# Performance work log

Measured on AMD Instinct MI355X. Metric: run time of the kernel, lower is better.

The kernel has to match this reference:

```python
import jax, jax.numpy as jnp
import numpy as np

DIM = 1024
DEPTH = 4
D_STATE = 16
D_CONV = 4
D_INNER = 2 * DIM
DT_RANK = (DIM + 15) // 16  # 64, ceil(dim/16) as in mamba-ssm
B_SZ, L = 4, 2048


def setup_inputs() -> dict:
    key = jax.random.key(0)
    ks = jax.random.split(key, 10)
    s = 0.02
    x = jax.random.normal(ks[0], (B_SZ, L, DIM), jnp.float32)
    in_proj_w = jax.random.normal(ks[1], (DEPTH, 2 * D_INNER, DIM), jnp.float32) * s
    conv_w = jax.random.normal(ks[2], (DEPTH, D_INNER, D_CONV), jnp.float32) * 0.2
    conv_b = jnp.zeros((DEPTH, D_INNER), jnp.float32)
    x_proj_w = jax.random.normal(ks[3], (DEPTH, DT_RANK + 2 * D_STATE, D_INNER), jnp.float32) * s
    dt_proj_w = jax.random.normal(ks[4], (DEPTH, D_INNER, DT_RANK), jnp.float32) * s
    # bias init so softplus(bias) ~ 0.01 (mamba dt_init)
    dt_proj_b = jnp.full((DEPTH, D_INNER), float(np.log(np.expm1(0.01))), jnp.float32)
    # S4D-real init: A = -(1..d_state)
    A_log = jnp.broadcast_to(jnp.log(jnp.arange(1, D_STATE + 1, dtype=jnp.float32)), (D_INNER, D_STATE))
    A_log = jnp.broadcast_to(A_log, (DEPTH, D_INNER, D_STATE))
    D = jnp.ones((DEPTH, D_INNER), jnp.float32)
    out_proj_w = jax.random.normal(ks[5], (DEPTH, DIM, D_INNER), jnp.float32) * s
    return {"x": x, "in_proj_w": in_proj_w, "conv_w": conv_w, "conv_b": conv_b,
            "x_proj_w": x_proj_w, "dt_proj_w": dt_proj_w, "dt_proj_b": dt_proj_b,
            "A_log": A_log, "D": D, "out_proj_w": out_proj_w}


def _selective_scan(u, delta, A, Bm, Cm, D):
    # u, delta: [B, L, d_inner]; Bm, Cm: [B, L, d_state]; A: [d_inner, d_state]
    def step(h, inp):
        u_t, d_t, b_t, c_t = inp  # [B,di], [B,di], [B,ds], [B,ds]
        dA = jnp.exp(d_t[:, :, None] * A)                 # [B,di,ds]
        h = dA * h + (d_t * u_t)[:, :, None] * b_t[:, None, :]
        y = jnp.einsum('bds,bs->bd', h, c_t)
        return h, y

    h0 = jnp.zeros((u.shape[0], u.shape[2], A.shape[1]), u.dtype)
    xs = (u.transpose(1, 0, 2), delta.transpose(1, 0, 2),
          Bm.transpose(1, 0, 2), Cm.transpose(1, 0, 2))
    _, ys = jax.lax.scan(step, h0, xs)                     # ys: [L,B,di]
    return ys.transpose(1, 0, 2) + u * D


def _mamba_layer(x, in_w, cw, cb, xp_w, dtw, dtb, A_log, D, ow):
    xz = jnp.einsum('bld,ed->ble', x, in_w)               # [B,L,2*di]
    xi, z = jnp.split(xz, 2, axis=-1)
    # causal depthwise conv over L
    xc = jax.lax.conv_general_dilated(
        xi.transpose(0, 2, 1),                             # [B,di,L]
        cw[:, None, :],                                    # [di,1,k]
        window_strides=(1,), padding=[(D_CONV - 1, 0)],
        feature_group_count=D_INNER,
        dimension_numbers=('NCH', 'OIH', 'NCH'))
    xc = jax.nn.silu(xc.transpose(0, 2, 1) + cb)           # [B,L,di]
    dbc = jnp.einsum('bld,ed->ble', xc, xp_w)              # [B,L,dt_rank+2*ds]
    dt, Bm, Cm = jnp.split(dbc, [DT_RANK, DT_RANK + D_STATE], axis=-1)
    delta = jax.nn.softplus(jnp.einsum('blr,dr->bld', dt, dtw) + dtb)
    A = -jnp.exp(A_log)
    y = _selective_scan(xc, delta, A, Bm, Cm, D)
    y = y * jax.nn.silu(z)
    return jnp.einsum('bld,od->blo', y, ow)


def reference(x, in_proj_w, conv_w, conv_b, x_proj_w, dt_proj_w, dt_proj_b, A_log, D, out_proj_w):
    for i in range(DEPTH):
        x = _mamba_layer(x, in_proj_w[i], conv_w[i], conv_b[i], x_proj_w[i],
                         dt_proj_w[i], dt_proj_b[i], A_log[i], D[i], out_proj_w[i])
    return x
```

## Files before the change

kernel.cpp:

```cpp
#include <hip/hip_runtime.h>
#include <hip/hip_bf16.h>
#include <math.h>

#define DIMK 1024
#define NDEPTH 4
#define DS 16
#define DCONV 4
#define DI 2048
#define DTR 64
#define NB 4
#define SL 2048
#define MT (NB * SL)
#define NXZ (2 * DI)
#define NDBC (DTR + 2 * DS)

typedef float f32x4 __attribute__((ext_vector_type(4)));
typedef short short8 __attribute__((ext_vector_type(8)));
typedef short short4v __attribute__((ext_vector_type(4)));

__device__ inline unsigned short f2bf(float f) {
    unsigned u = __builtin_bit_cast(unsigned, f);
    unsigned r = (u + 0x7FFFu + ((u >> 16) & 1u)) >> 16;
    return (unsigned short)r;
}
__device__ inline float bf2f(unsigned short h) {
    unsigned u = ((unsigned)h) << 16;
    return __builtin_bit_cast(float, u);
}
__device__ inline void split_bf(float f, unsigned short& hi, unsigned short& lo) {
    hi = f2bf(f);
    lo = f2bf(f - bf2f(hi));
}
__device__ inline unsigned short cvt1(float f) {
    __hip_bfloat16 t = __float2bfloat16(f);
    return __builtin_bit_cast(unsigned short, t);
}
__device__ inline void mfma16(f32x4& d, short8 a, short8 b) {
    asm volatile("v_mfma_f32_16x16x32_bf16 %0, %1, %2, %0"
                 : "+v"(d) : "v"(a), "v"(b));
}
__device__ __forceinline__ float dpp_sum16(float p) {
    asm("v_add_f32_dpp %0, %0, %0 quad_perm:[1,0,3,2] row_mask:0xf bank_mask:0xf bound_ctrl:0" : "+v"(p));
    asm("v_add_f32_dpp %0, %0, %0 quad_perm:[2,3,0,1] row_mask:0xf bank_mask:0xf bound_ctrl:0" : "+v"(p));
    asm("v_add_f32_dpp %0, %0, %0 row_ror:4 row_mask:0xf bank_mask:0xf bound_ctrl:0" : "+v"(p));
    asm("v_add_f32_dpp %0, %0, %0 row_ror:8 row_mask:0xf bank_mask:0xf bound_ctrl:0" : "+v"(p));
    return p;
}
__device__ __forceinline__ float exp2_raw(float x) {
    float r;
    asm("v_exp_f32 %0, %1" : "=v"(r) : "v"(x));
    return r;
}
__device__ __forceinline__ void gload16(const unsigned short* g, unsigned short* l) {
    __builtin_amdgcn_global_load_lds(
        (const __attribute__((address_space(1))) unsigned int*)(g),
        (__attribute__((address_space(3))) unsigned int*)(l),
        16, 0, 0);
}

__global__ __launch_bounds__(256) void cvt_bf16(
    const float* __restrict__ s, unsigned short* __restrict__ d, int n4)
{
    const int g = blockIdx.x * 256 + threadIdx.x;
    if (g < n4) {
        const float4 f = *(const float4*)(s + (size_t)g * 4);
        short4v v;
        v[0] = (short)cvt1(f.x); v[1] = (short)cvt1(f.y);
        v[2] = (short)cvt1(f.z); v[3] = (short)cvt1(f.w);
        *(short4v*)(d + (size_t)g * 4) = v;
    }
}

__global__ __launch_bounds__(256) void cvt_layer(
    const float* __restrict__ wi, const float* __restrict__ owp,
    const float* __restrict__ dtwp, const float* __restrict__ xpwp,
    unsigned short* __restrict__ wi16, unsigned short* __restrict__ ow16,
    unsigned short* __restrict__ dtwh, unsigned short* __restrict__ dtwl,
    unsigned short* __restrict__ xpwh, unsigned short* __restrict__ xpwl,
    int fastd, int fastx)
{
    int g = blockIdx.x * 256 + threadIdx.x;
    const int n4w = NXZ * DIMK / 4;
    const int n4o = DIMK * DI / 4;
    const int n4d = DI * DTR / 4;
    const int n4x = NDBC * DI / 4;
    if (g < n4w) {
        const float4 f = *(const float4*)(wi + (size_t)g * 4);
        short4v v;
        v[0] = (short)cvt1(f.x); v[1] = (short)cvt1(f.y);
        v[2] = (short)cvt1(f.z); v[3] = (short)cvt1(f.w);
        *(short4v*)(wi16 + (size_t)g * 4) = v;
        return;
    }
    g -= n4w;
    if (g < n4o) {
        const float4 f = *(const float4*)(owp + (size_t)g * 4);
        short4v v;
        v[0] = (short)cvt1(f.x); v[1] = (short)cvt1(f.y);
        v[2] = (short)cvt1(f.z); v[3] = (short)cvt1(f.w);
        *(short4v*)(ow16 + (size_t)g * 4) = v;
        return;
    }
    g -= n4o;
    if (g < n4d) {
        if (fastd) {
            const float4 f = *(const float4*)(dtwp + (size_t)g * 4);
            short4v h4, l4;
            #pragma unroll
            for (int e = 0; e < 4; ++e) {
                unsigned short h, l;
                split_bf((&f.x)[e], h, l);
                h4[e] = (short)h; l4[e] = (short)l;
            }
            *(short4v*)(dtwh + (size_t)g * 4) = h4;
            *(short4v*)(dtwl + (size_t)g * 4) = l4;
        }
        return;
    }
    g -= n4d;
    if (g < n4x && fastx) {
        const float4 f = *(const float4*)(xpwp + (size_t)g * 4);
        short4v h4, l4;
        #pragma unroll
        for (int e = 0; e < 4; ++e) {
            unsigned short h, l;
            split_bf((&f.x)[e], h, l);
            h4[e] = (short)h; l4[e] = (short)l;
        }
        *(short4v*)(xpwh + (size_t)g * 4) = h4;
        *(short4v*)(xpwl + (size_t)g * 4) = l4;
    }
}

template <int CBF>
__global__ __launch_bounds__(256) void gemm_bb(
    const unsigned short* __restrict__ A, const unsigned short* __restrict__ B,
    void* __restrict__ Cv, int K, int lda, int ldb, int ldc)
{
    __shared__ unsigned short As[2][128 * 32];
    __shared__ unsigned short Bs[2][128 * 32];
    int id = blockIdx.y * gridDim.x + blockIdx.x;
    const int qq = (gridDim.x * gridDim.y) >> 3;
    id = (id & 7) * qq + (id >> 3);
    const int bm = (id / gridDim.x) * 128, bn = (id % gridDim.x) * 128;

    const int tid = threadIdx.x;
    const int wv = tid >> 6, ln = tid & 63;
    const int wr = wv >> 1, wc = wv & 1;
    const int fr = ln & 15, kg = ln >> 4;
    const int sr0 = wv * 32 + (ln >> 2);
    const int sr1 = sr0 + 16;
    const int sl = ln & 3;
    const int cg0 = sl ^ ((sr0 >> 1) & 3);
    const int cg1 = sl ^ ((sr1 >> 1) & 3);
    const unsigned short* pa0 = A + (size_t)(bm + sr0) * lda + cg0 * 8;
    const unsigned short* pa1 = A + (size_t)(bm + sr1) * lda + cg1 * 8;
    const unsigned short* pb0 = B + (size_t)(bn + sr0) * ldb + cg0 * 8;
    const unsigned short* pb1 = B + (size_t)(bn + sr1) * ldb + cg1 * 8;
    const int ldst0 = (wv * 32 + 0) * 32;
    const int ldst1 = (wv * 32 + 16) * 32;
    int offA[4], offB[4];
    #pragma unroll
    for (int f = 0; f < 4; ++f) {
        const int ra = wr * 64 + f * 16 + fr;
        offA[f] = ra * 32 + ((kg ^ ((ra >> 1) & 3)) * 8);
        const int rb = wc * 64 + f * 16 + fr;
        offB[f] = rb * 32 + ((kg ^ ((rb >> 1) & 3)) * 8);
    }
    f32x4 acc[4][4] = {};
    gload16(pa0, &As[0][ldst0]);
    gload16(pa1, &As[0][ldst1]);
    gload16(pb0, &Bs[0][ldst0]);
    gload16(pb1, &Bs[0][ldst1]);
    __syncthreads();
    int cur = 0;
    for (int k0 = 0; k0 < K; k0 += 32) {
        const int nxt = cur ^ 1;
        if (k0 + 32 < K) {
            gload16(pa0 + k0 + 32, &As[nxt][ldst0]);
            gload16(pa1 + k0 + 32, &As[nxt][ldst1]);
            gload16(pb0 + k0 + 32, &Bs[nxt][ldst0]);
            gload16(pb1 + k0 + 32, &Bs[nxt][ldst1]);
        }
        short8 af[4], bw[4];
        #pragma unroll
        for (int f = 0; f < 4; ++f) {
            af[f] = *(const short8*)&As[cur][offA[f]];
            bw[f] = *(const short8*)&Bs[cur][offB[f]];
        }
        #pragma unroll
        for (int fi = 0; fi < 4; ++fi)
            #pragma unroll
            for (int fj = 0; fj < 4; ++fj)
                mfma16(acc[fi][fj], af[fi], bw[fj]);
        __syncthreads();
        cur = nxt;
    }
    #pragma unroll
    for (int fi = 0; fi < 4; ++fi) {
        const int m0 = bm + wr * 64 + fi * 16 + kg * 4;
        #pragma unroll
        for (int fj = 0; fj < 4; ++fj) {
            const int n = bn + wc * 64 + fj * 16 + fr;
            #pragma unroll
            for (int q = 0; q < 4; ++q) {
                if (CBF) {
                    unsigned short* Cs = (unsigned short*)Cv;
                    Cs[(size_t)(m0 + q) * ldc + n] = cvt1(acc[fi][fj][q]);
                } else {
                    float* Cf = (float*)Cv;
                    Cf[(size_t)(m0 + q) * ldc + n] = acc[fi][fj][q];
                }
            }
        }
    }
}

template <int CBF>
__global__ __launch_bounds__(256) void gemm_fb(
    const float* __restrict__ A, const unsigned short* __restrict__ B,
    void* __restrict__ Cv, int K, int lda, int ldb, int ldc)
{
    __shared__ unsigned short As[2][128 * 32];
    __shared__ unsigned short Bs[2][128 * 32];
    int id = blockIdx.y * gridDim.x + blockIdx.x;
    const int qq = (gridDim.x * gridDim.y) >> 3;
    id = (id & 7) * qq + (id >> 3);
    const int bm = (id / gridDim.x) * 128, bn = (id % gridDim.x) * 128;

    const int tid = threadIdx.x;
    const int wv = tid >> 6, ln = tid & 63;
    const int wr = wv >> 1, wc = wv & 1;
    const int fr = ln & 15, kg = ln >> 4;
    const int r = tid >> 1, hf = tid & 1;
    const int sr0 = wv * 32 + (ln >> 2);
    const int sr1 = sr0 + 16;
    const int sl = ln & 3;
    const int cg0 = sl ^ ((sr0 >> 1) & 3);
    const int cg1 = sl ^ ((sr1 >> 1) & 3);
    const unsigned short* pb0 = B + (size_t)(bn + sr0) * ldb + cg0 * 8;
    const unsigned short* pb1 = B + (size_t)(bn + sr1) * ldb + cg1 * 8;
    const int ldst0 = (wv * 32 + 0) * 32;
    const int ldst1 = (wv * 32 + 16) * 32;
    const float* ga = A + (size_t)(bm + r) * lda + hf * 16;
    const int pk0 = (2 * hf + 0) ^ ((r >> 1) & 3);
    const int pk1 = (2 * hf + 1) ^ ((r >> 1) & 3);
    int offA[4], offB[4];
    #pragma unroll
    for (int f = 0; f < 4; ++f) {
        const int ra = wr * 64 + f * 16 + fr;
        offA[f] = ra * 32 + ((kg ^ ((ra >> 1) & 3)) * 8);
        const int rb = wc * 64 + f * 16 + fr;
        offB[f] = rb * 32 + ((kg ^ ((rb >> 1) & 3)) * 8);
    }
    f32x4 acc[4][4] = {};
    {
        float4 f0 = *(const float4*)(ga + 0);
        float4 f1 = *(const float4*)(ga + 4);
        float4 f2 = *(const float4*)(ga + 8);
        float4 f3 = *(const float4*)(ga + 12);
        short8 v;
        v[0] = (short)cvt1(f0.x); v[1] = (short)cvt1(f0.y);
        v[2] = (short)cvt1(f0.z); v[3] = (short)cvt1(f0.w);
        v[4] = (short)cvt1(f1.x); v[5] = (short)cvt1(f1.y);
        v[6] = (short)cvt1(f1.z); v[7] = (short)cvt1(f1.w);
        *(short8*)&As[0][r * 32 + pk0 * 8] = v;
        v[0] = (short)cvt1(f2.x); v[1] = (short)cvt1(f2.y);
        v[2] = (short)cvt1(f2.z); v[3] = (short)cvt1(f2.w);
        v[4] = (short)cvt1(f3.x); v[5] = (short)cvt1(f3.y);
        v[6] = (short)cvt1(f3.z); v[7] = (short)cvt1(f3.w);
        *(short8*)&As[0][r * 32 + pk1 * 8] = v;
        gload16(pb0, &Bs[0][ldst0]);
        gload16(pb1, &Bs[0][ldst1]);
    }
    __syncthreads();
    int cur = 0;
    for (int k0 = 0; k0 < K; k0 += 32) {
        const int nxt = cur ^ 1;
        const bool more = (k0 + 32 < K);
        float4 f0, f1, f2, f3;
        if (more) {
            gload16(pb0 + k0 + 32, &Bs[nxt][ldst0]);
            gload16(pb1 + k0 + 32, &Bs[nxt][ldst1]);
            f0 = *(const float4*)(ga + k0 + 32);
            f1 = *(const float4*)(ga + k0 + 36);
            f2 = *(const float4*)(ga + k0 + 40);
            f3 = *(const float4*)(ga + k0 + 44);
        }
        short8 af[4], bw[4];
        #pragma unroll
        for (int f = 0; f < 4; ++f) {
            af[f] = *(const short8*)&As[cur][offA[f]];
            bw[f] = *(const short8*)&Bs[cur][offB[f]];
        }
        #pragma unroll
        for (int fi = 0; fi < 4; ++fi)
            #pragma unroll
            for (int fj = 0; fj < 4; ++fj)
                mfma16(acc[fi][fj], af[fi], bw[fj]);
        if (more) {
            short8 v;
            v[0] = (short)cvt1(f0.x); v[1] = (short)cvt1(f0.y);
            v[2] = (short)cvt1(f0.z); v[3] = (short)cvt1(f0.w);
            v[4] = (short)cvt1(f1.x); v[5] = (short)cvt1(f1.y);
            v[6] = (short)cvt1(f1.z); v[7] = (short)cvt1(f1.w);
            *(short8*)&As[nxt][r * 32 + pk0 * 8] = v;
            v[0] = (short)cvt1(f2.x); v[1] = (short)cvt1(f2.y);
            v[2] = (short)cvt1(f2.z); v[3] = (short)cvt1(f2.w);
            v[4] = (short)cvt1(f3.x); v[5] = (short)cvt1(f3.y);
            v[6] = (short)cvt1(f3.z); v[7] = (short)cvt1(f3.w);
            *(short8*)&As[nxt][r * 32 + pk1 * 8] = v;
        }
        __syncthreads();
        cur = nxt;
    }
    #pragma unroll
    for (int fi = 0; fi < 4; ++fi) {
        const int m0 = bm + wr * 64 + fi * 16 + kg * 4;
        #pragma unroll
        for (int fj = 0; fj < 4; ++fj) {
            const int n = bn + wc * 64 + fj * 16 + fr;
            #pragma unroll
            for (int q = 0; q < 4; ++q) {
                if (CBF) {
                    unsigned short* Cs = (unsigned short*)Cv;
                    Cs[(size_t)(m0 + q) * ldc + n] = cvt1(acc[fi][fj][q]);
                } else {
                    float* Cf = (float*)Cv;
                    Cf[(size_t)(m0 + q) * ldc + n] = acc[fi][fj][q];
                }
            }
        }
    }
}

__global__ __launch_bounds__(256) void gemm_mfma(
    const float* __restrict__ A, const float* __restrict__ W,
    float* __restrict__ C, int K, int lda, int ldc)
{
    __shared__ unsigned short As[128 * 32];
    __shared__ unsigned short Ws[128 * 32];
    const int tid = threadIdx.x;
    const int bm = blockIdx.y * 128;
    const int bn = blockIdx.x * 128;
    const int r = tid >> 1;
    const int h = tid & 1;
    const int wv = tid >> 6;
    const int wr = wv >> 1;
    const int wc = wv & 1;
// ... 342 lines not shown
        const int dst = (wv * 32 + j * 8) * 64;
        gload16(Ahg + (size_t)(bm + row) * DTR + scol, sAh + dst);
        gload16(Alg + (size_t)(bm + row) * DTR + scol, sAl + dst);
        gload16(Whg + (size_t)(bn + row) * DTR + scol, sWh + dst);
        gload16(Wlg + (size_t)(bn + row) * DTR + scol, sWl + dst);
    }
    __syncthreads();
    f32x4 acc[4][4] = {};
    #pragma unroll
    for (int ks = 0; ks < 2; ++ks) {
        short8 ah[4], alo[4], bh[4], bl[4];
        #pragma unroll
        for (int f = 0; f < 4; ++f) {
            const int ra = wr * 64 + f * 16 + fr;
            const int ao = ra * 64 + ks * 32 + ((kg ^ ((ra >> 1) & 3)) * 8);
            ah[f]  = *(const short8*)&sAh[ao];
            alo[f] = *(const short8*)&sAl[ao];
            const int rb = wc * 64 + f * 16 + fr;
            const int bo = rb * 64 + ks * 32 + ((kg ^ ((rb >> 1) & 3)) * 8);
            bh[f] = *(const short8*)&sWh[bo];
            bl[f] = *(const short8*)&sWl[bo];
        }
        #pragma unroll
        for (int fi = 0; fi < 4; ++fi)
            #pragma unroll
            for (int fj = 0; fj < 4; ++fj) {
                mfma16(acc[fi][fj], ah[fi], bh[fj]);
                mfma16(acc[fi][fj], ah[fi], bl[fj]);
                mfma16(acc[fi][fj], alo[fi], bh[fj]);
            }
    }
    #pragma unroll
    for (int fi = 0; fi < 4; ++fi) {
        const int m0 = bm + wr * 64 + fi * 16 + kg * 4;
        #pragma unroll
        for (int fj = 0; fj < 4; ++fj) {
            const int n = bn + wc * 64 + fj * 16 + fr;
            const float bb = bias[n];
            #pragma unroll
            for (int q = 0; q < 4; ++q) {
                float v = acc[fi][fj][q] + bb;
                v = (v > 20.f) ? v : log1pf(__expf(v));
                C[(size_t)(m0 + q) * NXZ + n] = v;
            }
        }
    }
}

__global__ __launch_bounds__(256) void conv_silu(
    const float* __restrict__ xz, const float* __restrict__ cw,
    const float* __restrict__ cb, float* __restrict__ xc)
{
    const int g = blockIdx.x * 256 + threadIdx.x;
    const int c4 = g & (DI / 4 - 1);
    const int mq = g >> 9;
    const int m0 = mq << 2;
    const int l0 = m0 & (SL - 1);
    const int c = c4 << 2;
    const float4 w0 = *(const float4*)(cw + (size_t)(c + 0) * DCONV);
    const float4 w1 = *(const float4*)(cw + (size_t)(c + 1) * DCONV);
    const float4 w2 = *(const float4*)(cw + (size_t)(c + 2) * DCONV);
    const float4 w3 = *(const float4*)(cw + (size_t)(c + 3) * DCONV);
    const float4 cb4 = *(const float4*)(cb + c);
    float4 x[7];
    #pragma unroll
    for (int i = 0; i < 7; ++i) {
        if (l0 - 3 + i >= 0)
            x[i] = *(const float4*)(xz + (size_t)(m0 - 3 + i) * NXZ + c);
        else
            x[i] = make_float4(0.f, 0.f, 0.f, 0.f);
    }
    #pragma unroll
    for (int j = 0; j < 4; ++j) {
        float4 acc = cb4;
        #pragma unroll
        for (int k = 0; k < DCONV; ++k) {
            const float4 v = x[j + k];
            acc.x = fmaf(v.x, (&w0.x)[k], acc.x);
            acc.y = fmaf(v.y, (&w1.x)[k], acc.y);
            acc.z = fmaf(v.z, (&w2.x)[k], acc.z);
            acc.w = fmaf(v.w, (&w3.x)[k], acc.w);
        }
        acc.x = acc.x / (1.f + __expf(-acc.x));
        acc.y = acc.y / (1.f + __expf(-acc.y));
        acc.z = acc.z / (1.f + __expf(-acc.z));
        acc.w = acc.w / (1.f + __expf(-acc.w));
        *(float4*)(xc + (size_t)(m0 + j) * DI + c) = acc;
    }
}

__global__ __launch_bounds__(256) void conv_silu_split(
    const float* __restrict__ xz, const float* __restrict__ cw,
    const float* __restrict__ cb, unsigned short* __restrict__ xch,
    unsigned short* __restrict__ xcl)
{
    const int g = blockIdx.x * 256 + threadIdx.x;
    const int c4 = g & (DI / 4 - 1);
    const int mq = g >> 9;
    const int m0 = mq << 2;
    const int l0 = m0 & (SL - 1);
    const int c = c4 << 2;
    const float4 w0 = *(const float4*)(cw + (size_t)(c + 0) * DCONV);
    const float4 w1 = *(const float4*)(cw + (size_t)(c + 1) * DCONV);
    const float4 w2 = *(const float4*)(cw + (size_t)(c + 2) * DCONV);
    const float4 w3 = *(const float4*)(cw + (size_t)(c + 3) * DCONV);
    const float4 cb4 = *(const float4*)(cb + c);
    float4 x[7];
    #pragma unroll
    for (int i = 0; i < 7; ++i) {
        if (l0 - 3 + i >= 0)
            x[i] = *(const float4*)(xz + (size_t)(m0 - 3 + i) * NXZ + c);
        else
            x[i] = make_float4(0.f, 0.f, 0.f, 0.f);
    }
    #pragma unroll
    for (int j = 0; j < 4; ++j) {
        float4 acc = cb4;
        #pragma unroll
        for (int k = 0; k < DCONV; ++k) {
            const float4 v = x[j + k];
            acc.x = fmaf(v.x, (&w0.x)[k], acc.x);
            acc.y = fmaf(v.y, (&w1.x)[k], acc.y);
            acc.z = fmaf(v.z, (&w2.x)[k], acc.z);
            acc.w = fmaf(v.w, (&w3.x)[k], acc.w);
        }
        short4v h4, l4;
        #pragma unroll
        for (int e = 0; e < 4; ++e) {
            float a = (&acc.x)[e];
            a = a / (1.f + __expf(-a));
            unsigned short hh, llo;
            split_bf(a, hh, llo);
            h4[e] = (short)hh; l4[e] = (short)llo;
        }
        *(short4v*)(xch + (size_t)(m0 + j) * DI + c) = h4;
        *(short4v*)(xcl + (size_t)(m0 + j) * DI + c) = l4;
    }
}

template <int YBF, int UBF>
__global__ __launch_bounds__(256) void scan_k(
    const float* uf, const unsigned short* __restrict__ uh,
    const unsigned short* __restrict__ ul,
    const float* __restrict__ dbc,
    const float* __restrict__ xz, void* __restrict__ yv,
    const float* __restrict__ Alog, const float* __restrict__ Dl)
{
    const int b = blockIdx.y;
    const int c0 = blockIdx.x * 16;
    const int tid = threadIdx.x;
    const int ch = tid >> 4;
    const int s = tid & 15;
    const float Aa = -__expf(Alog[(size_t)(c0 + ch) * DS + s]) * 1.44269504088896f;
    __shared__ float sdl[16][68];
    __shared__ float sxb[16][68];
    __shared__ float sbc[32][68];
    __shared__ float sy[2][64][16];
    __shared__ float sD[16];
    if (tid < 16) sD[tid] = Dl[c0 + tid];
    __syncthreads();
    float h = 0.f;
    const int row = tid >> 2;
    const int q = (tid & 3) << 2;
    int pp = 0;
    for (int t0b = 0; t0b < SL; t0b += 64) {
        const size_t mb = (size_t)b * SL + t0b;
        const float4 dlv = *(const float4*)(xz + (mb + row) * NXZ + c0 + q);
        float4 uv;
        if (UBF) {
            const short4v uh4 = *(const short4v*)(uh + (mb + row) * DI + c0 + q);
            const short4v ul4 = *(const short4v*)(ul + (mb + row) * DI + c0 + q);
            #pragma unroll
            for (int e = 0; e < 4; ++e)
                (&uv.x)[e] = bf2f((unsigned short)uh4[e]) +
                             bf2f((unsigned short)ul4[e]);
        } else {
            uv = *(const float4*)(uf + (mb + row) * DI + c0 + q);
        }
        const float4 zv = *(const float4*)(xz + (mb + row) * NXZ + DI + c0 + q);
        float4 p0, p1;
        #pragma unroll
        for (int j = 0; j < 4; ++j) {
            const float dl = (&dlv.x)[j], uu = (&uv.x)[j], zz = (&zv.x)[j];
            const float w = zz / (1.f + __expf(-zz));
            sdl[q + j][row] = dl;
            sxb[q + j][row] = dl * uu;
            (&p1.x)[j] = w;
            (&p0.x)[j] = uu * sD[q + j] * w;
        }
        #pragma unroll
        for (int p = 0; p < 2; ++p) {
            const int idx = p * 256 + tid;
            const int r2 = idx >> 3, q2 = (idx & 7) << 2;
            const float4 v = *(const float4*)(dbc + (mb + r2) * NDBC + DTR + q2);
            sbc[q2 + 0][r2] = v.x; sbc[q2 + 1][r2] = v.y;
            sbc[q2 + 2][r2] = v.z; sbc[q2 + 3][r2] = v.w;
        }
        __syncthreads();
        for (int it = 0; it < 16; ++it) {
            const int t0 = it * 4;
            const float4 dl4 = *(const float4*)&sdl[ch][t0];
            const float4 xb4 = *(const float4*)&sxb[ch][t0];
            const float4 B4  = *(const float4*)&sbc[s][t0];
            const float4 C4  = *(const float4*)&sbc[16 + s][t0];
            float py0, py1, py2, py3;
            {
                const float dA = exp2_raw(dl4.x * Aa);
                h = fmaf(dA, h, xb4.x * B4.x);
                py0 = dpp_sum16(h * C4.x);
            }
            {
                const float dA = exp2_raw(dl4.y * Aa);
                h = fmaf(dA, h, xb4.y * B4.y);
                py1 = dpp_sum16(h * C4.y);
            }
            {
                const float dA = exp2_raw(dl4.z * Aa);
                h = fmaf(dA, h, xb4.z * B4.z);
                py2 = dpp_sum16(h * C4.z);
            }
            {
                const float dA = exp2_raw(dl4.w * Aa);
                h = fmaf(dA, h, xb4.w * B4.w);
                py3 = dpp_sum16(h * C4.w);
            }
            if (s < 4) {
                const int t = t0 + s;
                const float lo_ = (s & 1) ? py1 : py0;
                const float hi_ = (s & 1) ? py3 : py2;
                sy[pp][t][ch] = (s & 2) ? hi_ : lo_;
            }
        }
        __syncthreads();
        if (YBF) {
            unsigned short* y16 = (unsigned short*)yv;
            short4v s4;
            #pragma unroll
            for (int e = 0; e < 4; ++e)
                s4[e] = (short)cvt1(fmaf(sy[pp][row][q + e],
                                         (&p1.x)[e], (&p0.x)[e]));
            *(short4v*)(y16 + (mb + row) * DI + c0 + q) = s4;
        } else {
            float* y = (float*)yv;
            float4 yvv;
            #pragma unroll
            for (int e = 0; e < 4; ++e)
                (&yvv.x)[e] = fmaf(sy[pp][row][q + e], (&p1.x)[e], (&p0.x)[e]);
            *(float4*)(y + (mb + row) * DI + c0 + q) = yvv;
        }
        pp ^= 1;
    }
}

extern "C" void kernel_launch(void* const* d_in, const int* in_sizes, int n_in,
                              void* d_out, int out_size, void* d_ws, size_t ws_size,
                              hipStream_t stream)
{
    const float* x0   = (const float*)d_in[0];
    const float* in_w = (const float*)d_in[1];
    const float* cw   = (const float*)d_in[2];
    const float* cb   = (const float*)d_in[3];
    const float* xpw  = (const float*)d_in[4];
    const float* dtw  = (const float*)d_in[5];
    const float* dtb  = (const float*)d_in[6];
    const float* Alog = (const float*)d_in[7];
    const float* Dp   = (const float*)d_in[8];
    const float* ow   = (const float*)d_in[9];

    const size_t perB = (size_t)SL * (NXZ + DI + NDBC) * sizeof(float);
    const size_t wby  = ((size_t)NXZ * DIMK + (size_t)DIMK * DI) * 2;
    int nbc = 0, fast = 0;
    if (ws_size >= 4 * perB + wby)      { nbc = 4; fast = 1; }
    else if (ws_size >= 2 * perB + wby) { nbc = 2; fast = 1; }
    else if (ws_size >= perB + wby)     { nbc = 1; fast = 1; }
    else if (ws_size >= 4 * perB)       { nbc = 4; }
    else if (ws_size >= 2 * perB)       { nbc = 2; }
    else if (ws_size >= perB)           { nbc = 1; }
    else return;
    const int nchunks = NB / nbc;
    const int M = nbc * SL;
    const size_t dtby = ((size_t)DI * DTR * 2 + (size_t)M * DTR * 2) * 2;
    const size_t yby  = (size_t)M * DI * 2;
    const size_t xpby = (size_t)NDBC * DI * 2 * 2;
    const size_t base = (size_t)nbc * perB + wby;
    const int fastd = fast && (ws_size >= base + dtby);
    const int fasty = fastd && (ws_size >= base + dtby + yby);
    const int fastx = fasty && (ws_size >= base + dtby + yby + xpby);

    float* xz  = (float*)d_ws;
    float* xc  = xz + (size_t)M * NXZ;
    float* dbc = xc + (size_t)M * DI;
    unsigned short* xch = (unsigned short*)xc;
    unsigned short* xcl = xch + (size_t)M * DI;
    unsigned short* wi16 = (unsigned short*)(dbc + (size_t)M * NDBC);
    unsigned short* ow16 = wi16 + (size_t)NXZ * DIMK;
    unsigned short* dtwh = ow16 + (size_t)DIMK * DI;
    unsigned short* dtwl = dtwh + (size_t)DI * DTR;
    unsigned short* dth  = dtwl + (size_t)DI * DTR;
    unsigned short* dtl  = dth + (size_t)M * DTR;
    unsigned short* y16  = dtl + (size_t)M * DTR;
    unsigned short* xpwh = y16 + (size_t)M * DI;
    unsigned short* xpwl = xpwh + (size_t)NDBC * DI;

    unsigned short* xb16 = (unsigned short*)d_out + (size_t)MT * DIMK;
    float* xbuf = (float*)d_out;

    const dim3 blk(256);
    if (fastx) {
        const int n4x = MT * DIMK / 4;
        cvt_bf16<<<dim3(n4x / 256), blk, 0, stream>>>(x0, xb16, n4x);
    }
    const int ncv = (NXZ * DIMK / 4) + (DIMK * DI / 4) + (DI * DTR / 4) +
                    (NDBC * DI / 4);
    for (int ly = 0; ly < NDEPTH; ++ly) {
        const float* Wi   = in_w + (size_t)ly * NXZ * DIMK;
        const float* cwl  = cw   + (size_t)ly * DI * DCONV;
        const float* cbl  = cb   + (size_t)ly * DI;
        const float* xpl  = xpw  + (size_t)ly * NDBC * DI;
        const float* dtwl_ = dtw + (size_t)ly * DI * DTR;
        const float* dtbl = dtb  + (size_t)ly * DI;
        const float* Al   = Alog + (size_t)ly * DI * DS;
        const float* Dl   = Dp   + (size_t)ly * DI;
        const float* owl  = ow   + (size_t)ly * DIMK * DI;

        if (fast)
            cvt_layer<<<dim3((ncv + 255) / 256), blk, 0, stream>>>(
                Wi, owl, dtwl_, xpl, wi16, ow16, dtwh, dtwl, xpwh, xpwl,
                fastd, fastx);

        for (int ck = 0; ck < nchunks; ++ck) {
            if (fastx) {
                const unsigned short* xin16 = xb16 + (size_t)ck * M * DIMK;
                gemm_bb<0><<<dim3(NXZ / 128, M / 128), blk, 0, stream>>>(
                    xin16, wi16, xz, DIMK, DIMK, DIMK, NXZ);
                conv_silu_split<<<dim3(M * (DI / 16) / 256), blk, 0, stream>>>(
                    xz, cwl, cbl, xch, xcl);
                gemm_xproj_pre<<<dim3(3, M / 128), blk, 0, stream>>>(
                    xch, xcl, xpwh, xpwl, dbc, dth, dtl);
                gemm_delta_pre<<<dim3(DI / 128, M / 128), blk, 0, stream>>>(
                    dth, dtl, dtwh, dtwl, xz, dtbl);
                scan_k<1, 1><<<dim3(DI / 16, nbc), blk, 0, stream>>>(
                    nullptr, xch, xcl, dbc, xz, y16, Al, Dl);
                void* dst = (ly < NDEPTH - 1)
                    ? (void*)(xb16 + (size_t)ck * M * DIMK)
                    : (void*)((float*)d_out + (size_t)ck * M * DIMK);
                if (ly < NDEPTH - 1)
                    gemm_bb<1><<<dim3(DIMK / 128, M / 128), blk, 0, stream>>>(
                        y16, ow16, dst, DI, DI, DI, DIMK);
                else
                    gemm_bb<0><<<dim3(DIMK / 128, M / 128), blk, 0, stream>>>(
                        y16, ow16, dst, DI, DI, DI, DIMK);
            } else if (fast) {
                if (ly == 0) {
                    const float* xin = x0 + (size_t)ck * M * DIMK;
                    gemm_fb<0><<<dim3(NXZ / 128, M / 128), blk, 0, stream>>>(
                        xin, wi16, xz, DIMK, DIMK, DIMK, NXZ);
                } else {
                    const unsigned short* xin16 = xb16 + (size_t)ck * M * DIMK;
                    gemm_bb<0><<<dim3(NXZ / 128, M / 128), blk, 0, stream>>>(
                        xin16, wi16, xz, DIMK, DIMK, DIMK, NXZ);
                }
                conv_silu<<<dim3(M * (DI / 16) / 256), blk, 0, stream>>>(
                    xz, cwl, cbl, xc);
                if (fastd) {
                    gemm_xproj<1><<<dim3(3, M / 128), blk, 0, stream>>>(
                        xc, xpl, dbc, DI, DI, dth, dtl);
                    gemm_delta_pre<<<dim3(DI / 128, M / 128), blk, 0, stream>>>(
                        dth, dtl, dtwh, dtwl, xz, dtbl);
                } else {
                    gemm_xproj<0><<<dim3(3, M / 128), blk, 0, stream>>>(
                        xc, xpl, dbc, DI, DI, nullptr, nullptr);
                    gemm_delta<<<dim3(DI / 128, M / 128), blk, 0, stream>>>(
                        dbc, dtwl_, xz, dtbl);
                }
                void* dst = (ly < NDEPTH - 1)
                    ? (void*)(xb16 + (size_t)ck * M * DIMK)
                    : (void*)((float*)d_out + (size_t)ck * M * DIMK);
                if (fasty) {
                    scan_k<1, 0><<<dim3(DI / 16, nbc), blk, 0, stream>>>(
                        xc, nullptr, nullptr, dbc, xz, y16, Al, Dl);
                    if (ly < NDEPTH - 1)
                        gemm_bb<1><<<dim3(DIMK / 128, M / 128), blk, 0, stream>>>(
                            y16, ow16, dst, DI, DI, DI, DIMK);
                    else
                        gemm_bb<0><<<dim3(DIMK / 128, M / 128), blk, 0, stream>>>(
                            y16, ow16, dst, DI, DI, DI, DIMK);
                } else {
                    scan_k<0, 0><<<dim3(DI / 16, nbc), blk, 0, stream>>>(
                        xc, nullptr, nullptr, dbc, xz, xc, Al, Dl);
                    if (ly < NDEPTH - 1)
                        gemm_fb<1><<<dim3(DIMK / 128, M / 128), blk, 0, stream>>>(
                            xc, ow16, dst, DI, DI, DI, DIMK);
                    else
                        gemm_fb<0><<<dim3(DIMK / 128, M / 128), blk, 0, stream>>>(
                            xc, ow16, dst, DI, DI, DI, DIMK);
                }
            } else {
                const float* xin = (ly == 0 ? x0 : xbuf) + (size_t)ck * M * DIMK;
                gemm_mfma<<<dim3(NXZ / 128, M / 128), blk, 0, stream>>>(
                    xin, Wi, xz, DIMK, DIMK, NXZ);
                conv_silu<<<dim3(M * (DI / 16) / 256), blk, 0, stream>>>(
                    xz, cwl, cbl, xc);
                gemm_xproj<0><<<dim3(3, M / 128), blk, 0, stream>>>(
                    xc, xpl, dbc, DI, DI, nullptr, nullptr);
                gemm_delta<<<dim3(DI / 128, M / 128), blk, 0, stream>>>(
                    dbc, dtwl_, xz, dtbl);
                scan_k<0, 0><<<dim3(DI / 16, nbc), blk, 0, stream>>>(
                    xc, nullptr, nullptr, dbc, xz, xc, Al, Dl);
                float* xdst = (ly == NDEPTH - 1 ? (float*)d_out : xbuf) +
                              (size_t)ck * M * DIMK;
                gemm_mfma<<<dim3(DIMK / 128, M / 128), blk, 0, stream>>>(
                    xc, owl, xdst, DI, DI, DIMK);
            }
        }
    }
}
```

Before: 1.650 ms.

## Prefetch scan tiles with double-buffered LDS, batch weight conversion, single-buffer GEMM

The selective-scan kernel now keeps double-buffered shared tiles. It prefetches the next 64-step tile's global loads into registers and defers the previous tile's output write so both overlap the recurrence. The aim is to hide global memory latency in the serial scan. All layers' weights are converted to bf16 in one launch up front when workspace allows, replacing the per-layer conversion kernels. gemm_bb drops its LDS double buffering and loads synchronously each k-step, which halves its shared memory but exposes load latency.

```diff
diff --git a/kernel.cpp b/kernel.cpp
--- a/kernel.cpp
+++ b/kernel.cpp
@@ -132,13 +132,75 @@
     }
 }
 
+__global__ __launch_bounds__(256) void cvt_all(
+    const float* __restrict__ wi, const float* __restrict__ owp,
+    const float* __restrict__ dtwp, const float* __restrict__ xpwp,
+    unsigned short* __restrict__ wi16, unsigned short* __restrict__ ow16,
+    unsigned short* __restrict__ dtwh, unsigned short* __restrict__ dtwl,
+    unsigned short* __restrict__ xpwh, unsigned short* __restrict__ xpwl)
+{
+    const int n4w = NXZ * DIMK / 4;
+    const int n4o = DIMK * DI / 4;
+    const int n4d = DI * DTR / 4;
+    const int n4x = NDBC * DI / 4;
+    const int per = n4w + n4o + n4d + n4x;
+    int g = blockIdx.x * 256 + threadIdx.x;
+    const int ly = g / per;
+    if (ly >= NDEPTH) return;
+    g -= ly * per;
+    if (g < n4w) {
+        const float4 f = *(const float4*)(wi + (size_t)ly * NXZ * DIMK + (size_t)g * 4);
+        short4v v;
+        v[0] = (short)cvt1(f.x); v[1] = (short)cvt1(f.y);
+        v[2] = (short)cvt1(f.z); v[3] = (short)cvt1(f.w);
+        *(short4v*)(wi16 + (size_t)ly * NXZ * DIMK + (size_t)g * 4) = v;
+        return;
+    }
+    g -= n4w;
+    if (g < n4o) {
+        const float4 f = *(const float4*)(owp + (size_t)ly * DIMK * DI + (size_t)g * 4);
+        short4v v;
+        v[0] = (short)cvt1(f.x); v[1] = (short)cvt1(f.y);
+        v[2] = (short)cvt1(f.z); v[3] = (short)cvt1(f.w);
+        *(short4v*)(ow16 + (size_t)ly * DIMK * DI + (size_t)g * 4) = v;
+        return;
+    }
+    g -= n4o;
+    if (g < n4d) {
+        const float4 f = *(const float4*)(dtwp + (size_t)ly * DI * DTR + (size_t)g * 4);
+        short4v h4, l4;
+        #pragma unroll
+        for (int e = 0; e < 4; ++e) {
+            unsigned short h, l;
+            split_bf((&f.x)[e], h, l);
+            h4[e] = (short)h; l4[e] = (short)l;
+        }
+        *(short4v*)(dtwh + (size_t)ly * DI * DTR + (size_t)g * 4) = h4;
+        *(short4v*)(dtwl + (size_t)ly * DI * DTR + (size_t)g * 4) = l4;
+        return;
+    }
+    g -= n4d;
+    if (g < n4x) {
+        const float4 f = *(const float4*)(xpwp + (size_t)ly * NDBC * DI + (size_t)g * 4);
+        short4v h4, l4;
+        #pragma unroll
+        for (int e = 0; e < 4; ++e) {
+            unsigned short h, l;
+            split_bf((&f.x)[e], h, l);
+            h4[e] = (short)h; l4[e] = (short)l;
+        }
+        *(short4v*)(xpwh + (size_t)ly * NDBC * DI + (size_t)g * 4) = h4;
+        *(short4v*)(xpwl + (size_t)ly * NDBC * DI + (size_t)g * 4) = l4;
+    }
+}
+
 template <int CBF>
 __global__ __launch_bounds__(256) void gemm_bb(
     const unsigned short* __restrict__ A, const unsigned short* __restrict__ B,
     void* __restrict__ Cv, int K, int lda, int ldb, int ldc)
 {
-    __shared__ unsigned short As[2][128 * 32];
-    __shared__ unsigned short Bs[2][128 * 32];
+    __shared__ unsigned short As[128 * 32];
+    __shared__ unsigned short Bs[128 * 32];
     int id = blockIdx.y * gridDim.x + blockIdx.x;
     const int qq = (gridDim.x * gridDim.y) >> 3;
     id = (id & 7) * qq + (id >> 3);
@@ -157,8 +219,10 @@
     const unsigned short* pa1 = A + (size_t)(bm + sr1) * lda + cg1 * 8;
     const unsigned short* pb0 = B + (size_t)(bn + sr0) * ldb + cg0 * 8;
     const unsigned short* pb1 = B + (size_t)(bn + sr1) * ldb + cg1 * 8;
-    const int ldst0 = (wv * 32 + 0) * 32;
-    const int ldst1 = (wv * 32 + 16) * 32;
+    unsigned short* la0 = As + (wv * 32 + 0) * 32;
+    unsigned short* la1 = As + (wv * 32 + 16) * 32;
+    unsigned short* lb0 = Bs + (wv * 32 + 0) * 32;
+    unsigned short* lb1 = Bs + (wv * 32 + 16) * 32;
     int offA[4], offB[4];
     #pragma unroll
     for (int f = 0; f < 4; ++f) {
@@ -168,25 +232,17 @@
         offB[f] = rb * 32 + ((kg ^ ((rb >> 1) & 3)) * 8);
     }
     f32x4 acc[4][4] = {};
-    gload16(pa0, &As[0][ldst0]);
-    gload16(pa1, &As[0][ldst1]);
-    gload16(pb0, &Bs[0][ldst0]);
-    gload16(pb1, &Bs[0][ldst1]);
-    __syncthreads();
-    int cur = 0;
     for (int k0 = 0; k0 < K; k0 += 32) {
-        const int nxt = cur ^ 1;
-        if (k0 + 32 < K) {
-            gload16(pa0 + k0 + 32, &As[nxt][ldst0]);
-            gload16(pa1 + k0 + 32, &As[nxt][ldst1]);
-            gload16(pb0 + k0 + 32, &Bs[nxt][ldst0]);
-            gload16(pb1 + k0 + 32, &Bs[nxt][ldst1]);
-        }
+        gload16(pa0 + k0, la0);
+        gload16(pa1 + k0, la1);
+        gload16(pb0 + k0, lb0);
+        gload16(pb1 + k0, lb1);
+        __syncthreads();
         short8 af[4], bw[4];
         #pragma unroll
         for (int f = 0; f < 4; ++f) {
-            af[f] = *(const short8*)&As[cur][offA[f]];
-            bw[f] = *(const short8*)&Bs[cur][offB[f]];
+            af[f] = *(const short8*)&As[offA[f]];
+            bw[f] = *(const short8*)&Bs[offB[f]];
         }
         #pragma unroll
         for (int fi = 0; fi < 4; ++fi)
@@ -194,7 +250,6 @@
             for (int fj = 0; fj < 4; ++fj)
                 mfma16(acc[fi][fj], af[fi], bw[fj]);
         __syncthreads();
-        cur = nxt;
     }
     #pragma unroll
     for (int fi = 0; fi < 4; ++fi) {
@@ -843,57 +898,101 @@
     const int ch = tid >> 4;
     const int s = tid & 15;
     const float Aa = -__expf(Alog[(size_t)(c0 + ch) * DS + s]) * 1.44269504088896f;
-    __shared__ float sdl[16][68];
-    __shared__ float sxb[16][68];
-    __shared__ float sbc[32][68];
+    __shared__ float sdl[2][16][68];
+    __shared__ float sxb[2][16][68];
+    __shared__ float sbc[2][32][68];
     __shared__ float sy[2][64][16];
     __shared__ float sD[16];
     if (tid < 16) sD[tid] = Dl[c0 + tid];
-    __syncthreads();
     float h = 0.f;
     const int row = tid >> 2;
     const int q = (tid & 3) << 2;
+    const size_t base = (size_t)b * SL;
+    const int r2a = tid >> 3, q2a = (tid & 7) << 2;
+    const int r2b = 32 + (tid >> 3);
+
+    float4 dlv, zv, g0, g1, uvf;
+    short4v uh4, ul4;
+    {
+        const size_t m = base + row;
+        dlv = *(const float4*)(xz + m * NXZ + c0 + q);
+        if (UBF) {
+            uh4 = *(const short4v*)(uh + m * DI + c0 + q);
+            ul4 = *(const short4v*)(ul + m * DI + c0 + q);
+        } else {
+            uvf = *(const float4*)(uf + m * DI + c0 + q);
+        }
+        zv = *(const float4*)(xz + m * NXZ + DI + c0 + q);
+        g0 = *(const float4*)(dbc + (base + r2a) * NDBC + DTR + q2a);
+        g1 = *(const float4*)(dbc + (base + r2b) * NDBC + DTR + q2a);
+    }
+    float4 p0c, p1c, p0p, p1p;
     int pp = 0;
-    for (int t0b = 0; t0b < SL; t0b += 64) {
-        const size_t mb = (size_t)b * SL + t0b;
-        const float4 dlv = *(const float4*)(xz + (mb + row) * NXZ + c0 + q);
+    __syncthreads();
+    const int NT = SL / 64;
+    for (int tile = 0; tile < NT; ++tile) {
+        const int buf = tile & 1;
         float4 uv;
         if (UBF) {
-            const short4v uh4 = *(const short4v*)(uh + (mb + row) * DI + c0 + q);
-            const short4v ul4 = *(const short4v*)(ul + (mb + row) * DI + c0 + q);
             #pragma unroll
             for (int e = 0; e < 4; ++e)
                 (&uv.x)[e] = bf2f((unsigned short)uh4[e]) +
                              bf2f((unsigned short)ul4[e]);
-        } else {
-            uv = *(const float4*)(uf + (mb + row) * DI + c0 + q);
-        }
-        const float4 zv = *(const float4*)(xz + (mb + row) * NXZ + DI + c0 + q);
-        float4 p0, p1;
+        } else uv = uvf;
         #pragma unroll
         for (int j = 0; j < 4; ++j) {
             const float dl = (&dlv.x)[j], uu = (&uv.x)[j], zz = (&zv.x)[j];
             const float w = zz / (1.f + __expf(-zz));
-            sdl[q + j][row] = dl;
-            sxb[q + j][row] = dl * uu;
-            (&p1.x)[j] = w;
-            (&p0.x)[j] = uu * sD[q + j] * w;
-        }
-        #pragma unroll
-        for (int p = 0; p < 2; ++p) {
-            const int idx = p * 256 + tid;
-            const int r2 = idx >> 3, q2 = (idx & 7) << 2;
-            const float4 v = *(const float4*)(dbc + (mb + r2) * NDBC + DTR + q2);
-            sbc[q2 + 0][r2] = v.x; sbc[q2 + 1][r2] = v.y;
-            sbc[q2 + 2][r2] = v.z; sbc[q2 + 3][r2] = v.w;
-        }
+            sdl[buf][q + j][row] = dl;
+            sxb[buf][q + j][row] = dl * uu;
+            (&p1c.x)[j] = w;
+            (&p0c.x)[j] = uu * sD[q + j] * w;
+        }
+        sbc[buf][q2a + 0][r2a] = g0.x; sbc[buf][q2a + 1][r2a] = g0.y;
+        sbc[buf][q2a + 2][r2a] = g0.z; sbc[buf][q2a + 3][r2a] = g0.w;
+        sbc[buf][q2a + 0][r2b] = g1.x; sbc[buf][q2a + 1][r2b] = g1.y;
+        sbc[buf][q2a + 2][r2b] = g1.z; sbc[buf][q2a + 3][r2b] = g1.w;
         __syncthreads();
+        if (tile > 0) {
+            const size_t mp = base + (size_t)(tile - 1) * 64 + row;
+            if (YBF) {
+                unsigned short* y16 = (unsigned short*)yv;
+                short4v s4;
+                #pragma unroll
+                for (int e = 0; e < 4; ++e)
+                    s4[e] = (short)cvt1(fmaf(sy[pp ^ 1][row][q + e],
+                                             (&p1p.x)[e], (&p0p.x)[e]));
+                *(short4v*)(y16 + mp * DI + c0 + q) = s4;
+            } else {
+                float* y = (float*)yv;
+                float4 yvv;
+                #pragma unroll
+                for (int e = 0; e < 4; ++e)
+                    (&yvv.x)[e] = fmaf(sy[pp ^ 1][row][q + e],
+                                       (&p1p.x)[e], (&p0p.x)[e]);
+                *(float4*)(y + mp * DI + c0 + q) = yvv;
+            }
+        }
+        if (tile + 1 < NT) {
+            const size_t m = base + (size_t)(tile + 1) * 64 + row;
+            dlv = *(const float4*)(xz + m * NXZ + c0 + q);
+            if (UBF) {
+                uh4 = *(const short4v*)(uh + m * DI + c0 + q);
+                ul4 = *(const short4v*)(ul + m * DI + c0 + q);
+            } else {
+                uvf = *(const float4*)(uf + m * DI + c0 + q);
+            }
+            zv = *(const float4*)(xz + m * NXZ + DI + c0 + q);
+            const size_t mb2 = base + (size_t)(tile + 1) * 64;
+            g0 = *(const float4*)(dbc + (mb2 + r2a) * NDBC + DTR + q2a);
+            g1 = *(const float4*)(dbc + (mb2 + r2b) * NDBC + DTR + q2a);
+        }
         for (int it = 0; it < 16; ++it) {
             const int t0 = it * 4;
-            const float4 dl4 = *(const float4*)&sdl[ch][t0];
-            const float4 xb4 = *(const float4*)&sxb[ch][t0];
-            const float4 B4  = *(const float4*)&sbc[s][t0];
-            const float4 C4  = *(const float4*)&sbc[16 + s][t0];
+            const float4 dl4 = *(const float4*)&sdl[buf][ch][t0];
+            const float4 xb4 = *(const float4*)&sxb[buf][ch][t0];
+            const float4 B4  = *(const float4*)&sbc[buf][s][t0];
+            const float4 C4  = *(const float4*)&sbc[buf][16 + s][t0];
             float py0, py1, py2, py3;
             {
                 const float dA = exp2_raw(dl4.x * Aa);
@@ -922,24 +1021,29 @@
                 sy[pp][t][ch] = (s & 2) ? hi_ : lo_;
             }
         }
-        __syncthreads();
+        p0p = p0c; p1p = p1c;
+        pp ^= 1;
+    }
+    __syncthreads();
+    {
+        const size_t mp = base + (size_t)(NT - 1) * 64 + row;
         if (YBF) {
             unsigned short* y16 = (unsigned short*)yv;
             short4v s4;
             #pragma unroll
             for (int e = 0; e < 4; ++e)
-                s4[e] = (short)cvt1(fmaf(sy[pp][row][q + e],
-                                         (&p1.x)[e], (&p0.x)[e]));
-            *(short4v*)(y16 + (mb + row) * DI + c0 + q) = s4;
+                s4[e] = (short)cvt1(fmaf(sy[pp ^ 1][row][q + e],
+                                         (&p1p.x)[e], (&p0p.x)[e]));
+            *(short4v*)(y16 + mp * DI + c0 + q) = s4;
         } else {
             float* y = (float*)yv;
             float4 yvv;
             #pragma unroll
             for (int e = 0; e < 4; ++e)
-                (&yvv.x)[e] = fmaf(sy[pp][row][q + e], (&p1.x)[e], (&p0.x)[e]);
-            *(float4*)(y + (mb + row) * DI + c0 + q) = yvv;
-        }
-        pp ^= 1;
+                (&yvv.x)[e] = fmaf(sy[pp ^ 1][row][q + e],
+                                   (&p1p.x)[e], (&p0p.x)[e]);
+            *(float4*)(y + mp * DI + c0 + q) = yvv;
+        }
     }
 }
 
@@ -977,29 +1081,55 @@
     const int fastd = fast && (ws_size >= base + dtby);
     const int fasty = fastd && (ws_size >= base + dtby + yby);
     const int fastx = fasty && (ws_size >= base + dtby + yby + xpby);
+    const size_t wAll = ((size_t)NDEPTH * NXZ * DIMK + (size_t)NDEPTH * DIMK * DI +
+                         2 * (size_t)NDEPTH * DI * DTR + 2 * (size_t)NDEPTH * NDBC * DI) * 2;
+    const size_t chunkBy = (size_t)nbc * perB;
+    const int fastw = fastx &&
+        (ws_size >= chunkBy + wAll + (size_t)M * DTR * 2 * 2 + yby);
 
     float* xz  = (float*)d_ws;
     float* xc  = xz + (size_t)M * NXZ;
     float* dbc = xc + (size_t)M * DI;
     unsigned short* xch = (unsigned short*)xc;
     unsigned short* xcl = xch + (size_t)M * DI;
-    unsigned short* wi16 = (unsigned short*)(dbc + (size_t)M * NDBC);
-    unsigned short* ow16 = wi16 + (size_t)NXZ * DIMK;
-    unsigned short* dtwh = ow16 + (size_t)DIMK * DI;
-    unsigned short* dtwl = dtwh + (size_t)DI * DTR;
-    unsigned short* dth  = dtwl + (size_t)DI * DTR;
-    unsigned short* dtl  = dth + (size_t)M * DTR;
-    unsigned short* y16  = dtl + (size_t)M * DTR;
-    unsigned short* xpwh = y16 + (size_t)M * DI;
-    unsigned short* xpwl = xpwh + (size_t)NDBC * DI;
+
+    unsigned short* p = (unsigned short*)(dbc + (size_t)M * NDBC);
+    unsigned short *wi16, *ow16, *dtwh, *dtwl, *xpwh, *xpwl, *dth, *dtl, *y16;
+    size_t wiStride = 0, owStride = 0, dtwStride = 0, xpwStride = 0;
+    if (fastw) {
+        wi16 = p;                    p += (size_t)NDEPTH * NXZ * DIMK;
+        ow16 = p;                    p += (size_t)NDEPTH * DIMK * DI;
+        dtwh = p;                    p += (size_t)NDEPTH * DI * DTR;
+        dtwl = p;                    p += (size_t)NDEPTH * DI * DTR;
+        xpwh = p;                    p += (size_t)NDEPTH * NDBC * DI;
+        xpwl = p;                    p += (size_t)NDEPTH * NDBC * DI;
+        wiStride = (size_t)NXZ * DIMK; owStride = (size_t)DIMK * DI;
+        dtwStride = (size_t)DI * DTR;  xpwStride = (size_t)NDBC * DI;
+    } else {
+        wi16 = p;                    p += (size_t)NXZ * DIMK;
+        ow16 = p;                    p += (size_t)DIMK * DI;
+        dtwh = p;                    p += (size_t)DI * DTR;
+        dtwl = p;                    p += (size_t)DI * DTR;
+        xpwh = nullptr; xpwl = nullptr;
+    }
+    dth = p;                         p += (size_t)M * DTR;
+    dtl = p;                         p += (size_t)M * DTR;
+    y16 = p;                         p += (size_t)M * DI;
+    if (!fastw && fastx) { xpwh = p; p += (size_t)NDBC * DI; xpwl = p; }
 
     unsigned short* xb16 = (unsigned short*)d_out + (size_t)MT * DIMK;
     float* xbuf = (float*)d_out;
 
     const dim3 blk(256);
     if (fastx) {
-        const int n4x = MT * DIMK / 4;
-        cvt_bf16<<<dim3(n4x / 256), blk, 0, stream>>>(x0, xb16, n4x);
+        const int n4x0 = MT * DIMK / 4;
+        cvt_bf16<<<dim3(n4x0 / 256), blk, 0, stream>>>(x0, xb16, n4x0);
+    }
+    if (fastw) {
+        const int per = (NXZ * DIMK / 4) + (DIMK * DI / 4) + (DI * DTR / 4) +
+                        (NDBC * DI / 4);
+        cvt_all<<<dim3((NDEPTH * per + 255) / 256), blk, 0, stream>>>(
+            in_w, ow, dtw, xpw, wi16, ow16, dtwh, dtwl, xpwh, xpwl);
     }
     const int ncv = (NXZ * DIMK / 4) + (DIMK * DI / 4) + (DI * DTR / 4) +
                     (NDBC * DI / 4);
@@ -1014,22 +1144,29 @@
         const float* Dl   = Dp   + (size_t)ly * DI;
         const float* owl  = ow   + (size_t)ly * DIMK * DI;
 
-        if (fast)
+        const unsigned short* wi16L = wi16 + (size_t)ly * wiStride;
+        const unsigned short* ow16L = ow16 + (size_t)ly * owStride;
+        const unsigned short* dtwhL = dtwh + (size_t)ly * dtwStride;
+        const unsigned short* dtwlL = dtwl + (size_t)ly * dtwStride;
+        const unsigned short* xpwhL = fastx ? xpwh + (size_t)ly * xpwStride : nullptr;
+        const unsigned short* xpwlL = fastx ? xpwl + (size_t)ly * xpwStride : nullptr;
+
+        if (fast && !fastw)
             cvt_layer<<<dim3((ncv + 255) / 256), blk, 0, stream>>>(
-                Wi, owl, dtwl_, xpl, wi16, ow16, dtwh, dtwl, xpwh, xpwl,
-                fastd, fastx);
+                Wi, owl, dtwl_, xpl, wi16, ow16, dtwh, dtwl,
+                (unsigned short*)xpwh, (unsigned short*)xpwl, fastd, fastx);
 
         for (int ck = 0; ck < nchunks; ++ck) {
             if (fastx) {
                 const unsigned short* xin16 = xb16 + (size_t)ck * M * DIMK;
                 gemm_bb<0><<<dim3(NXZ / 128, M / 128), blk, 0, stream>>>(
-                    xin16, wi16, xz, DIMK, DIMK, DIMK, NXZ);
+                    xin16, wi16L, xz, DIMK, DIMK, DIMK, NXZ);
                 conv_silu_split<<<dim3(M * (DI / 16) / 256), blk, 0, stream>>>(
                     xz, cwl, cbl, xch, xcl);
                 gemm_xproj_pre<<<dim3(3, M / 128), blk, 0, stream>>>(
-                    xch, xcl, xpwh, xpwl, dbc, dth, dtl);
+                    xch, xcl, xpwhL, xpwlL, dbc, dth, dtl);
                 gemm_delta_pre<<<dim3(DI / 128, M / 128), blk, 0, stream>>>(
-                    dth, dtl, dtwh, dtwl, xz, dtbl);
+                    dth, dtl, dtwhL, dtwlL, xz, dtbl);
                 scan_k<1, 1><<<dim3(DI / 16, nbc), blk, 0, stream>>>(
                     nullptr, xch, xcl, dbc, xz, y16, Al, Dl);
                 void* dst = (ly < NDEPTH - 1)
@@ -1037,10 +1174,10 @@
                     : (void*)((float*)d_out + (size_t)ck * M * DIMK);
                 if (ly < NDEPTH - 1)
                     gemm_bb<1><<<dim3(DIMK / 128, M / 128), blk, 0, stream>>>(
-                        y16, ow16, dst, DI, DI, DI, DIMK);
+                        y16, ow16L, dst, DI, DI, DI, DIMK);
                 else
                     gemm_bb<0><<<dim3(DIMK / 128, M / 128), blk, 0, stream>>>(
-                        y16, ow16, dst, DI, DI, DI, DIMK);
+                        y16, ow16L, dst, DI, DI, DI, DIMK);
             } else if (fast) {
                 if (ly == 0) {
                     const float* xin = x0 + (size_t)ck * M * DIMK;
```

After: 1.597 ms. 1.03x faster.
